# Optimization experiments

Hardware: AMD Instinct MI355X
Metric: run time of the kernel (lower is better)

The kernel has to match this reference:

```python
import jax, jax.numpy as jnp
import numpy as np
import math

NUM_HEADS = 12


def _rope_tables(nph, npw, half_head_dim):
    # grid coords: x = column index, y = row index, flattened row-major
    rows = jnp.arange(nph, dtype=jnp.float32)
    cols = jnp.arange(npw, dtype=jnp.float32)
    gy, gx = jnp.meshgrid(rows, cols, indexing='ij')
    coords = jnp.stack([gx.ravel(), gy.ravel()], axis=1)  # [N, 2]
    cmin = coords.min(axis=0, keepdims=True)
    cmax = coords.max(axis=0, keepdims=True)
    nc = (coords - cmin) / (cmax - cmin + 1e-8)
    div = jnp.exp(jnp.arange(0, half_head_dim, 2, dtype=jnp.float32)
                  * (-(math.log(10000.0) / half_head_dim)))  # [half/2]
    px = nc[:, 0:1] * div  # [N, half/2]
    py = nc[:, 1:2] * div
    rep = lambda t: jnp.repeat(t, 2, axis=-1)  # interleave: even/odd slots get same value
    return rep(jnp.cos(px)), rep(jnp.sin(px)), rep(jnp.cos(py)), rep(jnp.sin(py))


def _apply_rope(t, cos_x, sin_x, cos_y, sin_y):
    # t: [B, H, N, Dh]; tables: [N, Dh//2] broadcast over B, H
    half = t.shape[-1] // 2
    tx, ty = t[..., :half], t[..., half:]
    rx = tx * cos_x + jnp.roll(tx, 1, axis=-1) * sin_x
    ry = ty * cos_y + jnp.roll(ty, 1, axis=-1) * sin_y
    return jnp.concatenate([rx, ry], axis=-1)


def setup_inputs() -> dict:
    key = jax.random.key(0)
    k1, k2, k3 = jax.random.split(key, 3)
    B, S, E = 32, 577, 768  # 24*24 patches + 1 CLS token
    x = jax.random.normal(k1, (B, S, E), dtype=jnp.float32)
    w_qkv = jax.random.normal(k2, (3 * E, E), dtype=jnp.float32) * 0.02
    w_proj = jax.random.normal(k3, (E, E), dtype=jnp.float32) * 0.02
    return {"x": x, "w_qkv": w_qkv, "w_proj": w_proj,
            "num_patches_h": 24, "num_patches_w": 24}


def reference(x, w_qkv, w_proj, num_patches_h, num_patches_w):
    B, S, E = x.shape
    H = NUM_HEADS
    Dh = E // H
    # QKV projection (bias=False)
    qkv = jnp.einsum('bse,fe->bsf', x, w_qkv).reshape(B, S, 3, H, Dh)
    qkv = jnp.transpose(qkv, (2, 0, 3, 1, 4))  # [3, B, H, S, Dh]
    q, k, v = qkv[0], qkv[1], qkv[2]
    # 2D RoPE on patch tokens only (CLS at position 0 unchanged)
    cx, sx, cy, sy = _rope_tables(num_patches_h, num_patches_w, Dh // 2)
    q_patch = _apply_rope(q[:, :, 1:], cx, sx, cy, sy)
    k_patch = _apply_rope(k[:, :, 1:], cx, sx, cy, sy)
    q = jnp.concatenate([q[:, :, :1], q_patch], axis=2)
    k = jnp.concatenate([k[:, :, :1], k_patch], axis=2)
    # scaled dot-product attention (standard backend, dropout=0)
    attn = jnp.einsum('bhqd,bhkd->bhqk', q, k) * (Dh ** -0.5)
    attn = jax.nn.softmax(attn, axis=-1)
    out = jnp.einsum('bhqk,bhkd->bhqd', attn, v)
    out = jnp.transpose(out, (0, 2, 1, 3)).reshape(B, S, E)
    return out @ w_proj.T
```

## Files before the change

kernel.cpp:

```cpp
#include <hip/hip_runtime.h>
#include <hip/hip_bf16.h>
#include <cstdint>


typedef __attribute__((ext_vector_type(8))) short bf16x8;
typedef __attribute__((ext_vector_type(4))) float f32x4;

#define MFMA16(a, b, c) __builtin_amdgcn_mfma_f32_16x16x32_bf16((a), (b), (c), 0, 0, 0)

#define S_LEN 577
#define NHEAD 12
#define DHEAD 64
#define EMB   768
#define F3    2304
#define NT_KV 10
#define BUFO  (128 * 32)

__device__ __forceinline__ void gload_lds16(const __hip_bfloat16* g, __hip_bfloat16* l) {
    __builtin_amdgcn_global_load_lds(
        (const __attribute__((address_space(1))) unsigned int*)g,
        (__attribute__((address_space(3))) unsigned int*)l, 16, 0, 0);
}

__device__ __forceinline__ uint4 cvt8_f32(float4 a, float4 b) {
    union { uint4 u; __hip_bfloat16 h[8]; } r;
    r.h[0] = __float2bfloat16(a.x); r.h[1] = __float2bfloat16(a.y);
    r.h[2] = __float2bfloat16(a.z); r.h[3] = __float2bfloat16(a.w);
    r.h[4] = __float2bfloat16(b.x); r.h[5] = __float2bfloat16(b.y);
    r.h[6] = __float2bfloat16(b.z); r.h[7] = __float2bfloat16(b.w);
    return r.u;
}

__device__ __forceinline__ uint4 load8_f32(const float* p) {
    return cvt8_f32(*(const float4*)p, *(const float4*)(p + 4));
}

__global__ __launch_bounds__(256) void cvt_f32_bf16(
    const float* __restrict__ src, __hip_bfloat16* __restrict__ dst, int n8)
{
    const int i = blockIdx.x * 256 + threadIdx.x;
    if (i < n8)
        *(uint4*)(dst + (size_t)i * 8) = load8_f32(src + (size_t)i * 8);
}

template<bool BF32, bool CF32>
__global__ __launch_bounds__(256) void gemm_a_dma(
    const __hip_bfloat16* __restrict__ A, int lda,
    const void* __restrict__ Bv, int ldb,
    void* __restrict__ Cv, int M, int N, int K)
{
    __shared__ __hip_bfloat16 As[2 * BUFO];
    __shared__ __hip_bfloat16 Bs[2 * BUFO];

    const int t      = threadIdx.x;
    const int l      = t & 63;
    const int w      = t >> 6;
    const int lane15 = l & 15;
    const int quad   = l >> 4;

    const int n0 = blockIdx.x * 128;
    const int m0 = blockIdx.y * 128;
    const int wm = (w >> 1) * 64;
    const int wn = (w & 1) * 64;

    const int srow   = t >> 2;
    const int schunk = t & 3;
    const int fsw    = (t >> 3) & 3;
    const int gchunk = schunk ^ fsw;

    int ar0 = m0 + srow;       if (ar0 > M - 1) ar0 = M - 1;
    int ar1 = m0 + 64 + srow;  if (ar1 > M - 1) ar1 = M - 1;
    const int br0 = n0 + srow;
    const int br1 = n0 + 64 + srow;

    const __hip_bfloat16* pa0 = A + (size_t)ar0 * lda + gchunk * 8;
    const __hip_bfloat16* pa1 = A + (size_t)ar1 * lda + gchunk * 8;
    const size_t b0off = (size_t)br0 * ldb + gchunk * 8;
    const size_t b1off = (size_t)br1 * ldb + gchunk * 8;

    __hip_bfloat16* lAs0 = As + srow * 32 + schunk * 8;
    __hip_bfloat16* lAs1 = As + (64 + srow) * 32 + schunk * 8;
    __hip_bfloat16* lBs0 = Bs + srow * 32 + schunk * 8;
    __hip_bfloat16* lBs1 = Bs + (64 + srow) * 32 + schunk * 8;

    const int rsw = (quad ^ ((lane15 >> 1) & 3)) * 8;

    f32x4 acc[4][4] = {};

    gload_lds16(pa0, lAs0);
    gload_lds16(pa1, lAs1);
    if constexpr (BF32) {
        *(uint4*)lBs0 = load8_f32((const float*)Bv + b0off);
        *(uint4*)lBs1 = load8_f32((const float*)Bv + b1off);
    } else {
        gload_lds16((const __hip_bfloat16*)Bv + b0off, lBs0);
        gload_lds16((const __hip_bfloat16*)Bv + b1off, lBs1);
    }
    __syncthreads();

#define GEMM_STEP(kn, CO, NO)                                                 \
    {                                                                         \
        float4 g0 = {}, g1 = {}, g2 = {}, g3 = {};                            \
        const bool has_next = (kn) < K;                                       \
        if (has_next) {                                                       \
            gload_lds16(pa0 + (kn), lAs0 + (NO));                             \
            gload_lds16(pa1 + (kn), lAs1 + (NO));                             \
            if constexpr (BF32) {                                             \
                const float* pb0 = (const float*)Bv + b0off + (kn);           \
                const float* pb1 = (const float*)Bv + b1off + (kn);           \
                g0 = *(const float4*)pb0; g1 = *(const float4*)(pb0 + 4);     \
                g2 = *(const float4*)pb1; g3 = *(const float4*)(pb1 + 4);     \
            } else {                                                          \
                gload_lds16((const __hip_bfloat16*)Bv + b0off + (kn), lBs0 + (NO)); \
                gload_lds16((const __hip_bfloat16*)Bv + b1off + (kn), lBs1 + (NO)); \
            }                                                                 \
        }                                                                     \
        bf16x8 a[4], b[4];                                                    \
        _Pragma("unroll")                                                     \
        for (int i = 0; i < 4; ++i)                                           \
            a[i] = *(const bf16x8*)(As + (CO) + (wm + i * 16 + lane15) * 32 + rsw); \
        _Pragma("unroll")                                                     \
        for (int j = 0; j < 4; ++j)                                           \
            b[j] = *(const bf16x8*)(Bs + (CO) + (wn + j * 16 + lane15) * 32 + rsw); \
        _Pragma("unroll")                                                     \
        for (int i = 0; i < 4; ++i)                                           \
            _Pragma("unroll")                                                 \
            for (int j = 0; j < 4; ++j)                                       \
                acc[i][j] = MFMA16(a[i], b[j], acc[i][j]);                    \
        if constexpr (BF32) {                                                 \
            if (has_next) {                                                   \
                *(uint4*)(lBs0 + (NO)) = cvt8_f32(g0, g1);                    \
                *(uint4*)(lBs1 + (NO)) = cvt8_f32(g2, g3);                    \
            }                                                                 \
        }                                                                     \
        __syncthreads();                                                      \
    }

    for (int k0 = 0; k0 < K; k0 += 64) {
        GEMM_STEP(k0 + 32, 0,    BUFO)
        GEMM_STEP(k0 + 64, BUFO, 0)
    }
#undef GEMM_STEP

    #pragma unroll
    for (int i = 0; i < 4; ++i) {
        #pragma unroll
        for (int r = 0; r < 4; ++r) {
            const int m = m0 + wm + i * 16 + quad * 4 + r;
            if (m < M) {
                #pragma unroll
                for (int j = 0; j < 4; ++j) {
                    const int n = n0 + wn + j * 16 + lane15;
                    if constexpr (CF32)
                        ((float*)Cv)[(size_t)m * N + n] = acc[i][j][r];
                    else
                        ((__hip_bfloat16*)Cv)[(size_t)m * N + n] = __float2bfloat16(acc[i][j][r]);
                }
            }
        }
    }
}

__global__ __launch_bounds__(256) void rope_kernel(__hip_bfloat16* __restrict__ qkv)
{
    const int p = blockIdx.x;
    const int b = blockIdx.y;
    const int l = threadIdx.x & 63;
    const int w = threadIdx.x >> 6;

    const int jj   = l & 31;
    const float i2 = (float)((jj >> 1) * 2);
    const float dv = __expf(-i2 * 0.28782313662425576f);
    const float inv = 1.0f / (23.0f + 1e-8f);
    const float cx = (float)(p % 24) * inv;
    const float cy = (float)(p / 24) * inv;
    const float ang = ((l < 32) ? cx : cy) * dv;
    const float c = __cosf(ang);
    const float s = __sinf(ang);
    const int nb = (l & 32) | ((jj + 31) & 31);

    const size_t rowbase = ((size_t)(b * S_LEN + 1 + p)) * F3;

    for (int pr = w; pr < 24; pr += 4) {
        const int part = pr / 12;
        const int h    = pr % 12;
        const size_t off = rowbase + (size_t)part * EMB + h * DHEAD + l;
        float v  = __bfloat162float(qkv[off]);
        float vp = __shfl(v, nb, 64);
        qkv[off] = __float2bfloat16(v * c + vp * s);
    }
}

__global__ __launch_bounds__(512) void attn_kernel(
    const __hip_bfloat16* __restrict__ qkv,
    __hip_bfloat16* __restrict__ attn_out, int ldo)
{
    __shared__ __hip_bfloat16 Qs[128][72];
    __shared__ __hip_bfloat16 Ks[64][72];
    __shared__ __hip_bfloat16 Vt[64][72];

    const int t      = threadIdx.x;
    const int l      = t & 63;
    const int w      = t >> 6;
    const int lane15 = l & 15;
    const int quad   = l >> 4;

    const int q0 = blockIdx.x * 128;
    const int h  = blockIdx.y;
    const int b  = blockIdx.z;

    const int krow = t >> 3, kseg = t & 7;
    const int vs   = t & 63, vdg = t >> 6;

    uint4 ku, vu;
    {
        int gk = krow; if (gk > S_LEN - 1) gk = S_LEN - 1;
        ku = ((const uint4*)(qkv + (size_t)(b * S_LEN + gk) * F3 + EMB + h * DHEAD))[kseg];
        int gv = vs;  if (gv > S_LEN - 1) gv = S_LEN - 1;
        vu = ((const uint4*)(qkv + (size_t)(b * S_LEN + gv) * F3 + 2 * EMB + h * DHEAD))[vdg];
    }

    {
        const int row = t >> 2, seg = t & 3;
        int gq = q0 + row; if (gq > S_LEN - 1) gq = S_LEN - 1;
        const uint4* src = (const uint4*)(qkv + (size_t)(b * S_LEN + gq) * F3 + h * DHEAD + seg * 16);
        uint4 u0 = src[0], u1 = src[1];
        const __hip_bfloat16* e0 = (const __hip_bfloat16*)&u0;
        const __hip_bfloat16* e1 = (const __hip_bfloat16*)&u1;
        #pragma unroll
        for (int i = 0; i < 8; ++i) {
            Qs[row][seg * 16 + i]     = __float2bfloat16(__bfloat162float(e0[i]) * 0.125f);
            Qs[row][seg * 16 + 8 + i] = __float2bfloat16(__bfloat162float(e1[i]) * 0.125f);
        }
    }
    __syncthreads();

    bf16x8 qf0 = *(const bf16x8*)&Qs[w * 16 + lane15][quad * 8];
    bf16x8 qf1 = *(const bf16x8*)&Qs[w * 16 + lane15][32 + quad * 8];

    f32x4 o[4] = {};
    float m_i = -3.0e38f;
    float l_i = 0.f;

    for (int ti = 0; ti < NT_KV; ++ti) {
        __syncthreads();
        *(uint4*)&Ks[krow][kseg * 8] = ku;
        {
            const __hip_bfloat16* e0 = (const __hip_bfloat16*)&vu;
            #pragma unroll
            for (int i = 0; i < 8; ++i)
                Vt[vdg * 8 + i][vs] = e0[i];
        }
        if (ti + 1 < NT_KV) {
            int gk = (ti + 1) * 64 + krow; if (gk > S_LEN - 1) gk = S_LEN - 1;
            ku = ((const uint4*)(qkv + (size_t)(b * S_LEN + gk) * F3 + EMB + h * DHEAD))[kseg];
            int gv = (ti + 1) * 64 + vs;  if (gv > S_LEN - 1) gv = S_LEN - 1;
            vu = ((const uint4*)(qkv + (size_t)(b * S_LEN + gv) * F3 + 2 * EMB + h * DHEAD))[vdg];
        }
        asm volatile("s_waitcnt lgkmcnt(0)" ::: "memory");
        __builtin_amdgcn_s_barrier();
        asm volatile("" ::: "memory");

        f32x4 sf[4];
        #pragma unroll
        for (int nt = 0; nt < 4; ++nt) {
            f32x4 z = {0.f, 0.f, 0.f, 0.f};
            bf16x8 k0f = *(const bf16x8*)&Ks[nt * 16 + lane15][quad * 8];
            bf16x8 k1f = *(const bf16x8*)&Ks[nt * 16 + lane15][32 + quad * 8];
            z = MFMA16(k0f, qf0, z);
            z = MFMA16(k1f, qf1, z);
            sf[nt] = z;
        }
        const int s0 = ti * 64;
        #pragma unroll
        for (int nt = 0; nt < 4; ++nt)
            #pragma unroll
            for (int r = 0; r < 4; ++r)
                if (s0 + nt * 16 + quad * 4 + r >= S_LEN) sf[nt][r] = -1e30f;

        float mx = fmaxf(fmaxf(sf[0][0], sf[0][1]), fmaxf(sf[0][2], sf[0][3]));
        #pragma unroll
        for (int nt = 1; nt < 4; ++nt)
            mx = fmaxf(mx, fmaxf(fmaxf(sf[nt][0], sf[nt][1]), fmaxf(sf[nt][2], sf[nt][3])));
        mx = fmaxf(mx, __shfl_xor(mx, 16, 64));
        mx = fmaxf(mx, __shfl_xor(mx, 32, 64));

        const float mnew  = fmaxf(m_i, mx);
        const float alpha = __expf(m_i - mnew);
        m_i = mnew;

        float sum = 0.f;
        #pragma unroll
        for (int nt = 0; nt < 4; ++nt) {
            #pragma unroll
            for (int r = 0; r < 4; ++r) {
                sf[nt][r] = __expf(sf[nt][r] - mnew);
                sum += sf[nt][r];
            }
        }
        sum += __shfl_xor(sum, 16, 64);
        sum += __shfl_xor(sum, 32, 64);
        l_i = l_i * alpha + sum;

        float af[4];
        #pragma unroll
        for (int r = 0; r < 4; ++r)
            af[r] = __shfl(alpha, quad * 4 + r, 64);
        #pragma unroll
        for (int ci = 0; ci < 4; ++ci)
            #pragma unroll
            for (int r = 0; r < 4; ++r)
                o[ci][r] *= af[r];

        #pragma unroll
        for (int nt = 0; nt < 4; ++nt)
            #pragma unroll
            for (int r = 0; r < 4; ++r)
                Qs[w * 16 + lane15][nt * 16 + quad * 4 + r] = __float2bfloat16(sf[nt][r]);
        asm volatile("s_waitcnt lgkmcnt(0)" ::: "memory");

        #pragma unroll
        for (int s32 = 0; s32 < 2; ++s32) {
            bf16x8 pa = *(const bf16x8*)&Qs[w * 16 + lane15][s32 * 32 + quad * 8];
            #pragma unroll
            for (int ci = 0; ci < 4; ++ci) {
                bf16x8 vb = *(const bf16x8*)&Vt[ci * 16 + lane15][s32 * 32 + quad * 8];
                o[ci] = MFMA16(pa, vb, o[ci]);
            }
        }
    }

    #pragma unroll
    for (int r = 0; r < 4; ++r) {
        const float lr = __shfl(l_i, quad * 4 + r, 64);
        const int q = q0 + w * 16 + quad * 4 + r;
        if (q < S_LEN) {
            const float rl = 1.0f / lr;
            #pragma unroll
            for (int ci = 0; ci < 4; ++ci) {
                attn_out[(size_t)(b * S_LEN + q) * ldo + h * DHEAD + ci * 16 + lane15] =
                    __float2bfloat16(o[ci][r] * rl);
            }
        }
    }
}

extern "C" void kernel_launch(void* const* d_in, const int* in_sizes, int n_in,
                              void* d_out, int out_size, void* d_ws, size_t ws_size,
                              hipStream_t stream) {
    const float* x      = (const float*)d_in[0];
    const float* w_qkv  = (const float*)d_in[1];
    const float* w_proj = (const float*)d_in[2];
    for (int i = 0; i < n_in; ++i) {
        if      (in_sizes[i] == 32 * S_LEN * EMB) x      = (const float*)d_in[i];
        else if (in_sizes[i] == F3 * EMB)         w_qkv  = (const float*)d_in[i];
        else if (in_sizes[i] == EMB * EMB)        w_proj = (const float*)d_in[i];
    }
    float* out = (float*)d_out;

    const int Mrows = 32 * S_LEN;
    const int NX    = Mrows * EMB;
    const int NWQ   = F3 * EMB;

    __hip_bfloat16* qkv = (__hip_bfloat16*)d_ws;
    __hip_bfloat16* xb  = (__hip_bfloat16*)d_out;
    __hip_bfloat16* wb  = xb + (size_t)NX;

    cvt_f32_bf16<<<NX / 8 / 256, 256, 0, stream>>>(x, xb, NX / 8);
    cvt_f32_bf16<<<NWQ / 8 / 256, 256, 0, stream>>>(w_qkv, wb, NWQ / 8);
    gemm_a_dma<false, false><<<dim3(F3 / 128, (Mrows + 127) / 128), 256, 0, stream>>>(
        xb, EMB, wb, EMB, qkv, Mrows, F3, EMB);
    rope_kernel<<<dim3(576, 32), 256, 0, stream>>>(qkv);
    attn_kernel<<<dim3((S_LEN + 127) / 128, NHEAD, 32), 512, 0, stream>>>(qkv, qkv, F3);
    gemm_a_dma<true, true><<<dim3(EMB / 128, (Mrows + 127) / 128), 256, 0, stream>>>(
        qkv, F3, w_proj, EMB, out, Mrows, EMB, EMB);
}
```

Baseline: 395.8 us.

## Triple-buffer GEMM LDS tiles with two-step-ahead DMA prefetch and fine-grained waitcnt

```diff
diff --git a/kernel.cpp b/kernel.cpp
--- a/kernel.cpp
+++ b/kernel.cpp
@@ -49,8 +49,8 @@
     const void* __restrict__ Bv, int ldb,
     void* __restrict__ Cv, int M, int N, int K)
 {
-    __shared__ __hip_bfloat16 As[2 * BUFO];
-    __shared__ __hip_bfloat16 Bs[2 * BUFO];
+    __shared__ __hip_bfloat16 As[3 * BUFO];
+    __shared__ __hip_bfloat16 Bs[3 * BUFO];
 
     const int t      = threadIdx.x;
     const int l      = t & 63;
@@ -87,58 +87,93 @@
 
     f32x4 acc[4][4] = {};
 
-    gload_lds16(pa0, lAs0);
-    gload_lds16(pa1, lAs1);
     if constexpr (BF32) {
-        *(uint4*)lBs0 = load8_f32((const float*)Bv + b0off);
-        *(uint4*)lBs1 = load8_f32((const float*)Bv + b1off);
+        float4 h0, h1, h2, h3;
+        {
+            const float* pb0 = (const float*)Bv + b0off;
+            const float* pb1 = (const float*)Bv + b1off;
+            h0 = *(const float4*)pb0; h1 = *(const float4*)(pb0 + 4);
+            h2 = *(const float4*)pb1; h3 = *(const float4*)(pb1 + 4);
+        }
+        gload_lds16(pa0, lAs0);
+        gload_lds16(pa1, lAs1);
+        gload_lds16(pa0 + 32, lAs0 + BUFO);
+        gload_lds16(pa1 + 32, lAs1 + BUFO);
+        *(uint4*)lBs0 = cvt8_f32(h0, h1);
+        *(uint4*)lBs1 = cvt8_f32(h2, h3);
+        asm volatile("s_waitcnt vmcnt(2) lgkmcnt(0)" ::: "memory");
     } else {
+        gload_lds16(pa0, lAs0);
+        gload_lds16(pa1, lAs1);
         gload_lds16((const __hip_bfloat16*)Bv + b0off, lBs0);
         gload_lds16((const __hip_bfloat16*)Bv + b1off, lBs1);
-    }
-    __syncthreads();
-
-#define GEMM_STEP(kn, CO, NO)                                                 \
+        gload_lds16(pa0 + 32, lAs0 + BUFO);
+        gload_lds16(pa1 + 32, lAs1 + BUFO);
+        gload_lds16((const __hip_bfloat16*)Bv + b0off + 32, lBs0 + BUFO);
+        gload_lds16((const __hip_bfloat16*)Bv + b1off + 32, lBs1 + BUFO);
+        asm volatile("s_waitcnt vmcnt(4) lgkmcnt(0)" ::: "memory");
+    }
+    __builtin_amdgcn_s_barrier();
+
+#define GEMM_STEP(KC, CO, NB, NA)                                             \
     {                                                                         \
+        const int ka = (KC) + 64;                                             \
+        const int kb = (KC) + 32;                                             \
+        const bool hasA = ka < K;                                             \
+        const bool hasB = kb < K;                                             \
         float4 g0 = {}, g1 = {}, g2 = {}, g3 = {};                            \
-        const bool has_next = (kn) < K;                                       \
-        if (has_next) {                                                       \
-            gload_lds16(pa0 + (kn), lAs0 + (NO));                             \
-            gload_lds16(pa1 + (kn), lAs1 + (NO));                             \
-            if constexpr (BF32) {                                             \
-                const float* pb0 = (const float*)Bv + b0off + (kn);           \
-                const float* pb1 = (const float*)Bv + b1off + (kn);           \
+        if constexpr (BF32) {                                                 \
+            if (hasB) {        \
+                const float* pb0 = (const float*)Bv + b0off + kb;             \
+                const float* pb1 = (const float*)Bv + b1off + kb;             \
                 g0 = *(const float4*)pb0; g1 = *(const float4*)(pb0 + 4);     \
                 g2 = *(const float4*)pb1; g3 = *(const float4*)(pb1 + 4);     \
-            } else {                                                          \
-                gload_lds16((const __hip_bfloat16*)Bv + b0off + (kn), lBs0 + (NO)); \
-                gload_lds16((const __hip_bfloat16*)Bv + b1off + (kn), lBs1 + (NO)); \
+            }                                                                 \
+            if (hasA) {                                                       \
+                gload_lds16(pa0 + ka, lAs0 + (NA) * BUFO);                    \
+                gload_lds16(pa1 + ka, lAs1 + (NA) * BUFO);                    \
+            }                                                                 \
+        } else {                                                              \
+            if (hasA) {                                                       \
+                gload_lds16(pa0 + ka, lAs0 + (NA) * BUFO);                    \
+                gload_lds16(pa1 + ka, lAs1 + (NA) * BUFO);                    \
+                gload_lds16((const __hip_bfloat16*)Bv + b0off + ka, lBs0 + (NA) * BUFO); \
+                gload_lds16((const __hip_bfloat16*)Bv + b1off + ka, lBs1 + (NA) * BUFO); \
             }                                                                 \
         }                                                                     \
         bf16x8 a[4], b[4];                                                    \
         _Pragma("unroll")                                                     \
         for (int i = 0; i < 4; ++i)                                           \
-            a[i] = *(const bf16x8*)(As + (CO) + (wm + i * 16 + lane15) * 32 + rsw); \
+            a[i] = *(const bf16x8*)(As + (CO) * BUFO + (wm + i * 16 + lane15) * 32 + rsw); \
         _Pragma("unroll")                                                     \
         for (int j = 0; j < 4; ++j)                                           \
-            b[j] = *(const bf16x8*)(Bs + (CO) + (wn + j * 16 + lane15) * 32 + rsw); \
+            b[j] = *(const bf16x8*)(Bs + (CO) * BUFO + (wn + j * 16 + lane15) * 32 + rsw); \
         _Pragma("unroll")                                                     \
         for (int i = 0; i < 4; ++i)                                           \
             _Pragma("unroll")                                                 \
             for (int j = 0; j < 4; ++j)                                       \
                 acc[i][j] = MFMA16(a[i], b[j], acc[i][j]);                    \
         if constexpr (BF32) {                                                 \
-            if (has_next) {                                                   \
-                *(uint4*)(lBs0 + (NO)) = cvt8_f32(g0, g1);                    \
-                *(uint4*)(lBs1 + (NO)) = cvt8_f32(g2, g3);                    \
+            if (hasB) {                                                       \
+                *(uint4*)(lBs0 + (NB) * BUFO) = cvt8_f32(g0, g1);             \
+                *(uint4*)(lBs1 + (NB) * BUFO) = cvt8_f32(g2, g3);             \
             }                                                                 \
         }                                                                     \
-        __syncthreads();                                                      \
-    }
-
-    for (int k0 = 0; k0 < K; k0 += 64) {
-        GEMM_STEP(k0 + 32, 0,    BUFO)
-        GEMM_STEP(k0 + 64, BUFO, 0)
+        if (hasA) {                                                           \
+            if constexpr (BF32)                                               \
+                asm volatile("s_waitcnt vmcnt(2) lgkmcnt(0)" ::: "memory");   \
+            else                                                              \
+                asm volatile("s_waitcnt vmcnt(4) lgkmcnt(0)" ::: "memory");   \
+        } else {                                                              \
+            asm volatile("s_waitcnt vmcnt(0) lgkmcnt(0)" ::: "memory");       \
+        }                                                                     \
+        __builtin_amdgcn_s_barrier();                                         \
+    }
+
+    for (int k0 = 0; k0 < K; k0 += 96) {
+        GEMM_STEP(k0,      0, 1, 2)
+        GEMM_STEP(k0 + 32, 1, 2, 0)
+        GEMM_STEP(k0 + 64, 2, 0, 1)
     }
 #undef GEMM_STEP
 
```

Result: no change. 389.0 us (-1.7%).
